# Performance work log

Measured on AMD Instinct MI355X. Metric: run time of the kernel, lower is better.

## Reference

```python
import jax, jax.numpy as jnp
import numpy as np

V, F, P = 1024, 2048, 8192
_EPS = 1e-12


def setup_inputs() -> dict:
    key = jax.random.key(0)
    kv, kf, kp = jax.random.split(key, 3)
    verts = jax.random.normal(kv, (V, 3), dtype=jnp.float32)
    faces = jax.random.randint(kf, (F, 3), 0, V, dtype=jnp.int32)
    points = jax.random.normal(kp, (P, 3), dtype=jnp.float32)
    return {"verts": verts, "faces": faces, "points": points}


def _closest_point_on_tri(p, a, b, c):
    """Ericson's closest-point-on-triangle, broadcast over leading dims.
    p, a, b, c: [..., 3] -> closest point [..., 3]."""
    ab = b - a
    ac = c - a
    ap = p - a
    d1 = jnp.sum(ab * ap, -1)
    d2 = jnp.sum(ac * ap, -1)
    bp = p - b
    d3 = jnp.sum(ab * bp, -1)
    d4 = jnp.sum(ac * bp, -1)
    cp = p - c
    d5 = jnp.sum(ab * cp, -1)
    d6 = jnp.sum(ac * cp, -1)
    vc = d1 * d4 - d3 * d2
    vb = d5 * d2 - d1 * d6
    va = d3 * d6 - d5 * d4
    # guarded edge/interior parameters (denominators are >0 whenever the
    # corresponding region condition holds; eps keeps unselected branches finite)
    t_ab = d1 / jnp.maximum(d1 - d3, _EPS)
    t_ac = d2 / jnp.maximum(d2 - d6, _EPS)
    t_bc = (d4 - d3) / jnp.maximum((d4 - d3) + (d5 - d6), _EPS)
    denom = jnp.maximum(va + vb + vc, _EPS)
    v_in = vb / denom
    w_in = vc / denom
    # first-match region selection (vertex A, vertex B, edge AB, vertex C, edge AC, edge BC, interior)
    cA = (d1 <= 0) & (d2 <= 0)
    cB = (d3 >= 0) & (d4 <= d3)
    cAB = (vc <= 0) & (d1 >= 0) & (d3 <= 0)
    cC = (d6 >= 0) & (d5 <= d6)
    cAC = (vb <= 0) & (d2 >= 0) & (d6 <= 0)
    cBC = (va <= 0) & ((d4 - d3) >= 0) & ((d5 - d6) >= 0)
    z = jnp.zeros_like(d1)
    o = jnp.ones_like(d1)
    bv = jnp.select([cA, cB, cAB, cC, cAC, cBC], [z, o, t_ab, z, z, 1.0 - t_bc], v_in)
    bw = jnp.select([cA, cB, cAB, cC, cAC, cBC], [z, z, z, o, t_ac, t_bc], w_in)
    bu = 1.0 - bv - bw
    return a * bu[..., None] + b * bv[..., None] + c * bw[..., None]


def reference(verts, faces, points):
    tri = verts[faces]  # [F, 3, 3]
    a = tri[:, 0][None]  # [1, F, 3]
    b = tri[:, 1][None]
    c = tri[:, 2][None]
    cp = _closest_point_on_tri(points[:, None, :], a, b, c)  # [P, F, 3]
    dist2 = jnp.sum((points[:, None, :] - cp) ** 2, -1)  # [P, F] squared distances
    assoc = jnp.argmin(dist2, axis=1).astype(jnp.int32)  # [P] nearest triangle index
    dist = jnp.min(dist2, axis=1)  # [P]
    # loss_type == 'mse': kernel loss = sum(dist), then *= 1000 / P
    loss = jnp.sum(dist) * (1000.0 / points.shape[0])
    return loss, dist, assoc
```

## Files before the change

kernel.cpp:

```cpp
#include <hip/hip_runtime.h>
#include <float.h>

#define P_TOTAL 8192
#define F_TOTAL 2048
#define TPB     256
#define CHUNK   256
#define NCHUNK  (F_TOTAL / CHUNK)

__device__ __forceinline__ float refine_rcp(float D) {
#pragma clang fp contract(off)
    float r0 = __builtin_amdgcn_rcpf(D);
    float e1 = __builtin_fmaf(-D, r0, 1.0f);
    return __builtin_fmaf(e1, r0, r0);
}
__device__ __forceinline__ float div_rn(float num, float D, float r) {
#pragma clang fp contract(off)
    float q0 = num * r;
    float e  = __builtin_fmaf(-D, q0, num);
    return __builtin_fmaf(e, r, q0);
}

__device__ __forceinline__ void region_select(
    float d1, float d2, float d3, float d4, float d5, float d6,
    float va, float vb, float vc, float d43, float d56,
    float g1, float g2, float g3, float g4,
    float& bu, float& bv, float& bw)
{
#pragma clang fp contract(off)
    float G1 = fmaxf(g1, 1e-12f);
    float G2 = fmaxf(g2, 1e-12f);
    float G3 = fmaxf(g3, 1e-12f);
    float G4 = fmaxf(g4, 1e-12f);

    bool cA  = (d1 <= 0.f) & (d2 <= 0.f);
    bool cB  = (d3 >= 0.f) & (d4 <= d3);
    bool cAB = (vc <= 0.f) & (d1 >= 0.f) & (d3 <= 0.f);
    bool cC  = (d6 >= 0.f) & (d5 <= d6);
    bool cAC = (vb <= 0.f) & (d2 >= 0.f) & (d6 <= 0.f);
    bool cBC = (va <= 0.f) & (d43 >= 0.f) & (d56 >= 0.f);

    float nv = cA ? 0.f : cB ? 1.f : cAB ? d1 : cC ? 0.f
             : cAC ? 0.f : cBC ? d43 : vb;
    float nw = cA ? 0.f : cB ? 0.f : cAB ? 0.f : cC ? 1.f
             : cAC ? d2 : cBC ? d43 : vc;
    float D  = cA ? 1.f : cB ? 1.f : cAB ? G1 : cC ? 1.f
             : cAC ? G2 : cBC ? G3 : G4;
    bool fBC = cBC && !(cA || cB || cAB || cC || cAC);

    float r   = refine_rcp(D);
    float qv  = div_rn(nv, D, r);
    float bww = div_rn(nw, D, r);
    float bvv = fBC ? (1.0f - qv) : qv;
    bv = bvv; bw = bww;
    bu = (1.0f - bvv) - bww;
}

__device__ __forceinline__ float eval_exact(
    float px, float py, float pz, float4 q0, float4 q1, float4 q2)
{
#pragma clang fp contract(off)
    float ax = q0.x, ay = q0.y, az = q0.z;
    float bx = q0.w, by = q1.x, bz = q1.y;
    float cx = q1.z, cy = q1.w, cz = q2.x;

    float abx = bx - ax, aby = by - ay, abz = bz - az;
    float acx = cx - ax, acy = cy - ay, acz = cz - az;
    float apx = px - ax, apy = py - ay, apz = pz - az;
    float d1 = (abx * apx + aby * apy) + abz * apz;
    float d2 = (acx * apx + acy * apy) + acz * apz;
    float bpx = px - bx, bpy = py - by, bpz = pz - bz;
    float d3 = (abx * bpx + aby * bpy) + abz * bpz;
    float d4 = (acx * bpx + acy * bpy) + acz * bpz;
    float cpx = px - cx, cpy = py - cy, cpz = pz - cz;
    float d5 = (abx * cpx + aby * cpy) + abz * cpz;
    float d6 = (acx * cpx + acy * cpy) + acz * cpz;

    float vc = d1 * d4 - d3 * d2;
    float vb = d5 * d2 - d1 * d6;
    float va = d3 * d6 - d5 * d4;
    float d43 = d4 - d3, d56 = d5 - d6;
    float g1 = d1 - d3, g2 = d2 - d6, g3 = d43 + d56, g4 = (va + vb) + vc;

    float bu, bv, bw;
    region_select(d1, d2, d3, d4, d5, d6, va, vb, vc, d43, d56,
                  g1, g2, g3, g4, bu, bv, bw);

    float cpx2 = (ax * bu + bx * bv) + cx * bw;
    float cpy2 = (ay * bu + by * bv) + cy * bw;
    float cpz2 = (az * bu + bz * bv) + cz * bw;
    float dx = px - cpx2, dy = py - cpy2, dz = pz - cpz2;
    return (dx * dx + dy * dy) + dz * dz;
}

__global__ __launch_bounds__(256) void msdf_prep(
    const float* __restrict__ verts, const int* __restrict__ faces,
    float4* __restrict__ pre_n, float4* __restrict__ pre_v,
    float4* __restrict__ pre_a)
{
    int t = blockIdx.x * 256 + threadIdx.x;
    int i0 = faces[3 * t + 0], i1 = faces[3 * t + 1], i2 = faces[3 * t + 2];
    float ax = verts[3 * i0], ay = verts[3 * i0 + 1], az = verts[3 * i0 + 2];
    float bx = verts[3 * i1], by = verts[3 * i1 + 1], bz = verts[3 * i1 + 2];
    float cx = verts[3 * i2], cy = verts[3 * i2 + 1], cz = verts[3 * i2 + 2];
    float e1x = bx - ax, e1y = by - ay, e1z = bz - az;
    float e2x = cx - ax, e2y = cy - ay, e2z = cz - az;
    float nx = e1y * e2z - e1z * e2y;
    float ny = e1z * e2x - e1x * e2z;
    float nz = e1x * e2y - e1y * e2x;
    float nn = (nx * nx + ny * ny) + nz * nz;
    float inv = (nn > 1e-30f) ? (1.0f / sqrtf(nn)) : 0.0f;
    nx *= inv; ny *= inv; nz *= inv;
    pre_n[t] = make_float4(nx, ny, nz, (nx * ax + ny * ay) + nz * az);
    pre_v[3 * t + 0] = make_float4(ax, ay, az, bx);
    pre_v[3 * t + 1] = make_float4(by, bz, cx, cy);
    pre_v[3 * t + 2] = make_float4(cz, 0.f, 0.f, 0.f);
    pre_a[t] = make_float4(ax, ay, az, 0.f);
}

__global__ __launch_bounds__(TPB) void msdf_main(
    const float4* __restrict__ pre_n, const float4* __restrict__ pre_v,
    const float4* __restrict__ pre_a,
    const float* __restrict__ points, float* __restrict__ out)
{
    __shared__ int slist[4][512];
    const int tid  = threadIdx.x;
    const int lane = tid & 63;
    const int w    = tid >> 6;
    const int p    = blockIdx.x * 4 + w;

    const float px = points[3 * p], py = points[3 * p + 1], pz = points[3 * p + 2];

    float u = FLT_MAX;
    #pragma unroll
    for (int s = 0; s < F_TOTAL / 64; ++s) {
        float4 q = pre_a[s * 64 + lane];
        float dx = px - q.x, dy = py - q.y, dz = pz - q.z;
        u = fminf(u, (dx * dx + dy * dy) + dz * dz);
    }
    #pragma unroll
    for (int off = 32; off; off >>= 1)
        u = fminf(u, __shfl_xor(u, off, 64));
    float ub = u;

    unsigned int best_bits = 0xFFFFFFFFu;
    int best_idx = 0;
    int pend = 0, h = 0;

    for (int c = 0; c < NCHUNK; ++c) {
        const float ubm = ub * 1.02f + 1e-18f;
        #pragma unroll
        for (int s = 0; s < 4; ++s) {
            int t = c * CHUNK + s * 64 + lane;
            float4 n = pre_n[t];
            float lv = ((n.x * px + n.y * py) + n.z * pz) - n.w;
            bool pred = (lv * lv <= ubm);
            unsigned long long m = __ballot(pred);
            if (pred) {
                int off = (int)__popcll(m & ((1ull << lane) - 1ull));
                slist[w][(h + pend + off) & 511] = t;
            }
            pend += (int)__popcll(m);
        }
        bool drain = (c == NCHUNK - 1);
        while (pend >= 64 || (drain && pend > 0)) {
            int n_ev = pend < 64 ? pend : 64;
            int j = (lane < n_ev) ? lane : 0;
            int t = slist[w][(h + j) & 511];
            float4 q0 = pre_v[3 * t + 0];
            float4 q1 = pre_v[3 * t + 1];
            float4 q2 = pre_v[3 * t + 2];
            float d2v = eval_exact(px, py, pz, q0, q1, q2);
            unsigned int bits = __float_as_uint(d2v);
            if (bits < best_bits) { best_bits = bits; best_idx = t; }
            float ubc = d2v;
            #pragma unroll
            for (int off = 32; off; off >>= 1)
                ubc = fminf(ubc, __shfl_xor(ubc, off, 64));
            ub = fminf(ub, ubc);
            h += n_ev; pend -= n_ev;
        }
    }

    unsigned long long key =
        ((unsigned long long)best_bits << 32) | (unsigned int)best_idx;
    #pragma unroll
    for (int off = 32; off > 0; off >>= 1) {
        unsigned int hi = (unsigned int)(key >> 32);
        unsigned int lo = (unsigned int)(key & 0xFFFFFFFFu);
        unsigned int ohi = __shfl_down(hi, off, 64);
        unsigned int olo = __shfl_down(lo, off, 64);
        unsigned long long ok = ((unsigned long long)ohi << 32) | olo;
        key = (ok < key) ? ok : key;
    }
    if (lane == 0) {
        out[1 + p]           = __uint_as_float((unsigned int)(key >> 32));
        out[1 + P_TOTAL + p] = (float)(unsigned int)(key & 0xFFFFFFFFu);
    }
}

__global__ __launch_bounds__(1024) void msdf_loss(float* __restrict__ out)
{
    __shared__ float wsum[16];
    float s = 0.f;
    #pragma unroll
    for (int k = 0; k < P_TOTAL / 1024; ++k)
        s += out[1 + k * 1024 + threadIdx.x];
    #pragma unroll
    for (int off = 32; off > 0; off >>= 1) s += __shfl_down(s, off, 64);
    int lane = threadIdx.x & 63, w = threadIdx.x >> 6;
    if (lane == 0) wsum[w] = s;
    __syncthreads();
    if (threadIdx.x == 0) {
        float tot = 0.f;
        #pragma unroll
        for (int i = 0; i < 16; ++i) tot += wsum[i];
        out[0] = tot * (1000.0f / (float)P_TOTAL);
    }
}

extern "C" void kernel_launch(void* const* d_in, const int* in_sizes, int n_in,
                              void* d_out, int out_size, void* d_ws, size_t ws_size,
                              hipStream_t stream) {
    const float* verts  = (const float*)d_in[0];
    const int*   faces  = (const int*)d_in[1];
    const float* points = (const float*)d_in[2];
    float* out = (float*)d_out;
    float4* pre_n = (float4*)d_ws;
    float4* pre_v = (float4*)((char*)d_ws + F_TOTAL * 16);
    float4* pre_a = (float4*)((char*)d_ws + F_TOTAL * 16 * 4);

    msdf_prep<<<dim3(F_TOTAL / 256), dim3(256), 0, stream>>>(verts, faces, pre_n, pre_v, pre_a);
    msdf_main<<<dim3(P_TOTAL / 4), dim3(TPB), 0, stream>>>(pre_n, pre_v, pre_a, points, out);
    msdf_loss<<<dim3(1), dim3(1024), 0, stream>>>(out);
}
```

Measured before the change: 96.46 us.

## Tighten bound early, then batch candidate culling with larger LDS queue

Processes the first 256 faces and fully evaluates them to get a tight upper bound, then scans the remaining faces with a fixed threshold, flushing only when the queue (now 1024 entries) nears full. The vertex-distance prepass is split into two independent accumulators for more ILP. This trades fewer threshold refreshes (possibly more candidates surviving culling) for fewer partial-batch flushes and divergent loop iterations.

```diff
diff --git a/kernel.cpp b/kernel.cpp
--- a/kernel.cpp
+++ b/kernel.cpp
@@ -4,8 +4,6 @@
 #define P_TOTAL 8192
 #define F_TOTAL 2048
 #define TPB     256
-#define CHUNK   256
-#define NCHUNK  (F_TOTAL / CHUNK)
 
 __device__ __forceinline__ float refine_rcp(float D) {
 #pragma clang fp contract(off)
@@ -117,12 +115,42 @@
     pre_a[t] = make_float4(ax, ay, az, 0.f);
 }
 
+#define FLUSH_BODY() do {                                                 \
+    int n_ev = pend < 64 ? pend : 64;                                     \
+    int j = (lane < n_ev) ? lane : 0;                                     \
+    int t = slist[w][(h + j) & 1023];                                     \
+    float4 q0 = pre_v[3 * t + 0];                                         \
+    float4 q1 = pre_v[3 * t + 1];                                         \
+    float4 q2 = pre_v[3 * t + 2];                                         \
+    float d2v = eval_exact(px, py, pz, q0, q1, q2);                       \
+    unsigned int bits = __float_as_uint(d2v);                             \
+    if (bits < best_bits) { best_bits = bits; best_idx = t; }             \
+    float ubc = d2v;                                                      \
+    for (int off = 32; off; off >>= 1)                                    \
+        ubc = fminf(ubc, __shfl_xor(ubc, off, 64));                       \
+    ub = fminf(ub, ubc);                                                  \
+    h += n_ev; pend -= n_ev;                                              \
+} while (0)
+
+#define PUSH_STEP(step) do {                                              \
+    int t = (step) * 64 + lane;                                           \
+    float4 n = pre_n[t];                                                  \
+    float lv = ((n.x * px + n.y * py) + n.z * pz) - n.w;                  \
+    bool pred = (lv * lv <= ubm);                                         \
+    unsigned long long m = __ballot(pred);                                \
+    if (pred) {                                                           \
+        int off = (int)__popcll(m & ((1ull << lane) - 1ull));             \
+        slist[w][(h + pend + off) & 1023] = t;                            \
+    }                                                                     \
+    pend += (int)__popcll(m);                                             \
+} while (0)
+
 __global__ __launch_bounds__(TPB) void msdf_main(
     const float4* __restrict__ pre_n, const float4* __restrict__ pre_v,
     const float4* __restrict__ pre_a,
     const float* __restrict__ points, float* __restrict__ out)
 {
-    __shared__ int slist[4][512];
+    __shared__ int slist[4][1024];
     const int tid  = threadIdx.x;
     const int lane = tid & 63;
     const int w    = tid >> 6;
@@ -130,13 +158,17 @@
 
     const float px = points[3 * p], py = points[3 * p + 1], pz = points[3 * p + 2];
 
-    float u = FLT_MAX;
-    #pragma unroll
-    for (int s = 0; s < F_TOTAL / 64; ++s) {
-        float4 q = pre_a[s * 64 + lane];
-        float dx = px - q.x, dy = py - q.y, dz = pz - q.z;
-        u = fminf(u, (dx * dx + dy * dy) + dz * dz);
-    }
+    float u0 = FLT_MAX, u1 = FLT_MAX;
+    #pragma unroll
+    for (int s = 0; s < 16; ++s) {
+        float4 qa = pre_a[(2 * s) * 64 + lane];
+        float4 qb = pre_a[(2 * s + 1) * 64 + lane];
+        float dax = px - qa.x, day = py - qa.y, daz = pz - qa.z;
+        float dbx = px - qb.x, dby = py - qb.y, dbz = pz - qb.z;
+        u0 = fminf(u0, (dax * dax + day * day) + daz * daz);
+        u1 = fminf(u1, (dbx * dbx + dby * dby) + dbz * dbz);
+    }
+    float u = fminf(u0, u1);
     #pragma unroll
     for (int off = 32; off; off >>= 1)
         u = fminf(u, __shfl_xor(u, off, 64));
@@ -146,40 +178,24 @@
     int best_idx = 0;
     int pend = 0, h = 0;
 
-    for (int c = 0; c < NCHUNK; ++c) {
-        const float ubm = ub * 1.02f + 1e-18f;
+    {
+        float ubm = ub * 1.02f + 1e-18f;
         #pragma unroll
-        for (int s = 0; s < 4; ++s) {
-            int t = c * CHUNK + s * 64 + lane;
-            float4 n = pre_n[t];
-            float lv = ((n.x * px + n.y * py) + n.z * pz) - n.w;
-            bool pred = (lv * lv <= ubm);
-            unsigned long long m = __ballot(pred);
-            if (pred) {
-                int off = (int)__popcll(m & ((1ull << lane) - 1ull));
-                slist[w][(h + pend + off) & 511] = t;
+        for (int s = 0; s < 4; ++s) PUSH_STEP(s);
+        while (pend > 0) FLUSH_BODY();
+    }
+
+    {
+        float ubm = ub * 1.02f + 1e-18f;
+        for (int s = 4; s < 32; ++s) {
+            PUSH_STEP(s);
+            if (pend >= 960) {
+                while (pend >= 64) FLUSH_BODY();
+                ubm = ub * 1.02f + 1e-18f;
             }
-            pend += (int)__popcll(m);
         }
-        bool drain = (c == NCHUNK - 1);
-        while (pend >= 64 || (drain && pend > 0)) {
-            int n_ev = pend < 64 ? pend : 64;
-            int j = (lane < n_ev) ? lane : 0;
-            int t = slist[w][(h + j) & 511];
-            float4 q0 = pre_v[3 * t + 0];
-            float4 q1 = pre_v[3 * t + 1];
-            float4 q2 = pre_v[3 * t + 2];
-            float d2v = eval_exact(px, py, pz, q0, q1, q2);
-            unsigned int bits = __float_as_uint(d2v);
-            if (bits < best_bits) { best_bits = bits; best_idx = t; }
-            float ubc = d2v;
-            #pragma unroll
-            for (int off = 32; off; off >>= 1)
-                ubc = fminf(ubc, __shfl_xor(ubc, off, 64));
-            ub = fminf(ub, ubc);
-            h += n_ev; pend -= n_ev;
-        }
-    }
+    }
+    while (pend > 0) FLUSH_BODY();
 
     unsigned long long key =
         ((unsigned long long)best_bits << 32) | (unsigned int)best_idx;
```

Result: no change. 98.04 us (+1.6%).
